# Kernel optimization log

Measured on AMD Instinct MI355X. Metric: run time of the kernel, lower is better.

## Reference

```python
import jax, jax.numpy as jnp
import numpy as np

B, S, HID = 2, 2048, 2048
NH, NKV, HD = 8, 2, 256
EPS = 1e-6
ROPE_THETA = 1e6


def _rms_norm(x, w):
    # Gemma3nRMSNorm: computed in fp32, x / sqrt(mean(x^2) + eps) * w
    xf = x.astype(jnp.float32)
    out = xf * jax.lax.rsqrt(jnp.mean(xf * xf, axis=-1, keepdims=True) + EPS) * w
    return out.astype(x.dtype)


def _rotate_half(x):
    x1, x2 = jnp.split(x, 2, axis=-1)
    return jnp.concatenate((-x2, x1), axis=-1)


def _apply_rope(x, cos, sin):
    # x: [B, S, H, D]; cos/sin: [B, S, D] -> unsqueeze head dim (unsqueeze_dim=2)
    c = cos[:, :, None, :]
    s = sin[:, :, None, :]
    return x * c + _rotate_half(x) * s


def setup_inputs() -> dict:
    key = jax.random.key(0)
    ks = jax.random.split(key, 6)
    hidden_states = jax.random.normal(ks[0], (B, S, HID), dtype=jnp.float32)
    # RoPE tables (theta = 1e6, Gemma3n)
    inv_freq = 1.0 / (ROPE_THETA ** (np.arange(0, HD, 2, dtype=np.float32) / HD))
    pos = np.arange(S, dtype=np.float32)
    freqs = pos[:, None] * inv_freq[None, :]            # [S, D/2]
    emb = np.concatenate([freqs, freqs], axis=-1)        # [S, D]
    cos = jnp.broadcast_to(jnp.asarray(np.cos(emb)), (B, S, HD)).astype(jnp.float32)
    sin = jnp.broadcast_to(jnp.asarray(np.sin(emb)), (B, S, HD)).astype(jnp.float32)
    # additive causal mask [B, 1, S, S]
    causal = jnp.tril(jnp.ones((S, S), dtype=bool))
    attention_mask = jnp.where(causal, 0.0, -1e9).astype(jnp.float32)
    attention_mask = jnp.broadcast_to(attention_mask[None, None], (B, 1, S, S))
    std = 0.02
    Wq = jax.random.normal(ks[1], (NH * HD, HID), dtype=jnp.float32) * std
    Wk = jax.random.normal(ks[2], (NKV * HD, HID), dtype=jnp.float32) * std
    Wv = jax.random.normal(ks[3], (NKV * HD, HID), dtype=jnp.float32) * std
    Wo = jax.random.normal(ks[4], (HID, NH * HD), dtype=jnp.float32) * std
    q_norm_w = jnp.ones((HD,), dtype=jnp.float32)
    k_norm_w = jnp.ones((HD,), dtype=jnp.float32)
    return {
        "hidden_states": hidden_states, "cos": cos, "sin": sin,
        "attention_mask": attention_mask,
        "Wq": Wq, "Wk": Wk, "Wv": Wv, "Wo": Wo,
        "q_norm_w": q_norm_w, "k_norm_w": k_norm_w,
    }


def reference(hidden_states, cos, sin, attention_mask, Wq, Wk, Wv, Wo, q_norm_w, k_norm_w):
    b, s, _ = hidden_states.shape
    # projections (no bias)
    q = (hidden_states @ Wq.T).reshape(b, s, NH, HD)
    k = (hidden_states @ Wk.T).reshape(b, s, NKV, HD)
    v = (hidden_states @ Wv.T).reshape(b, s, NKV, HD)
    # QK-norm then RoPE; v_norm has no scale (weight = 1)
    q = _apply_rope(_rms_norm(q, q_norm_w), cos, sin)
    k = _apply_rope(_rms_norm(k, k_norm_w), cos, sin)
    v = _rms_norm(v, jnp.float32(1.0))
    q = q.transpose(0, 2, 1, 3)  # [B, NH, S, D]
    k = k.transpose(0, 2, 1, 3)  # [B, NKV, S, D]
    v = v.transpose(0, 2, 1, 3)
    # repeat_kv: NKV -> NH (n_rep = NH // NKV)
    n_rep = NH // NKV
    k = jnp.repeat(k, n_rep, axis=1)
    v = jnp.repeat(v, n_rep, axis=1)
    # eager attention, scaling = 1.0 (as in Gemma3nTextAttention), no softcap
    scores = jnp.einsum("bhqd,bhkd->bhqk", q, k) + attention_mask
    probs = jax.nn.softmax(scores.astype(jnp.float32), axis=-1).astype(q.dtype)
    out = jnp.einsum("bhqk,bhkd->bqhd", probs, v).reshape(b, s, NH * HD)
    return out @ Wo.T
```

## Files before the change

kernel.cpp:

```cpp
#include <hip/hip_runtime.h>
#include <hip/hip_bf16.h>
#include <stdint.h>

#define S_LEN 2048
#define HIDN  2048
#define NH    8
#define NKV   2
#define HD    256

typedef _Float16 v8h  __attribute__((ext_vector_type(8)));
typedef float    v4f  __attribute__((ext_vector_type(4)));
typedef float    v16f __attribute__((ext_vector_type(16)));
typedef unsigned short u16;

struct alignas(8) US4 { u16 x, y, z, w; };

__device__ __forceinline__ u16 f2h(float f) {
  union { _Float16 h; u16 u; } t; t.h = (_Float16)f; return t.u;
}
__device__ __forceinline__ float h2f(u16 u) {
  union { _Float16 h; u16 u; } t; t.u = u; return (float)t.h;
}
__device__ __forceinline__ uint32_t pk2(float a, float b) {
  return (uint32_t)f2h(a) | ((uint32_t)f2h(b) << 16);
}

template <typename T>
__device__ __forceinline__ void gload16(const T* g, void* l) {
  __builtin_amdgcn_global_load_lds(
      (const __attribute__((address_space(1))) void*)g,
      (__attribute__((address_space(3))) void*)l, 16, 0, 0);
}

__global__ void cvt_h_kernel(const float* __restrict__ in, u16* __restrict__ out, int n4) {
  int i = blockIdx.x * blockDim.x + threadIdx.x;
  if (i >= n4) return;
  float4 v = reinterpret_cast<const float4*>(in)[i];
  US4 o; o.x = f2h(v.x); o.y = f2h(v.y); o.z = f2h(v.z); o.w = f2h(v.w);
  reinterpret_cast<US4*>(out)[i] = o;
}

__global__ __launch_bounds__(256, 2) void gemm_h_nt(
    const u16* __restrict__ A, const u16* __restrict__ Bm,
    float* __restrict__ C, int M, int N, int K) {
  __shared__ u16 As[128 * 32];
  __shared__ u16 Bs[128 * 32];
  const int tid = threadIdx.x;
  const int w = tid >> 6, lane = tid & 63;
  const int m0 = blockIdx.x * 128, n0 = blockIdx.y * 128;
  const int wr = (w >> 1) * 64, wc = (w & 1) * 64;
  const int lr = lane & 15, lk = (lane >> 4) << 3;
  v4f acc[4][4] = {};
  const int row1 = tid >> 2, col1 = (tid & 3) << 3;
  const int t2 = tid + 256;
  const int row2 = t2 >> 2, col2 = (t2 & 3) << 3;
  for (int kt = 0; kt < K; kt += 32) {
    __syncthreads();
    gload16(A  + (size_t)(m0 + row1) * K + kt + col1, (char*)As + tid * 16);
    gload16(Bm + (size_t)(n0 + row1) * K + kt + col1, (char*)Bs + tid * 16);
    gload16(A  + (size_t)(m0 + row2) * K + kt + col2, (char*)As + t2 * 16);
    gload16(Bm + (size_t)(n0 + row2) * K + kt + col2, (char*)Bs + t2 * 16);
    __syncthreads();
    v8h af[4], bfr[4];
#pragma unroll
    for (int i = 0; i < 4; i++) af[i]  = *reinterpret_cast<const v8h*>(&As[(wr + i * 16 + lr) * 32 + lk]);
#pragma unroll
    for (int i = 0; i < 4; i++) bfr[i] = *reinterpret_cast<const v8h*>(&Bs[(wc + i * 16 + lr) * 32 + lk]);
#pragma unroll
    for (int i = 0; i < 4; i++)
#pragma unroll
      for (int jn = 0; jn < 4; jn++)
        acc[i][jn] = __builtin_amdgcn_mfma_f32_16x16x32_f16(af[i], bfr[jn], acc[i][jn], 0, 0, 0);
  }
  const int rbase = m0 + wr + ((lane >> 4) << 2);
  const int cbase = n0 + wc + lr;
#pragma unroll
  for (int i = 0; i < 4; i++)
#pragma unroll
    for (int jn = 0; jn < 4; jn++) {
      const int col = cbase + jn * 16;
#pragma unroll
      for (int j = 0; j < 4; j++)
        C[(size_t)(rbase + i * 16 + j) * N + col] = acc[i][jn][j];
    }
}

__global__ __launch_bounds__(256, 4) void norm_rope_kernel(
    const float* __restrict__ qkv, const float* __restrict__ cosb, const float* __restrict__ sinb,
    const float* __restrict__ qw, const float* __restrict__ kw,
    u16* __restrict__ q_t, u16* __restrict__ k_t, u16* __restrict__ v_t) {
  const int task = blockIdx.x * 4 + (threadIdx.x >> 6);
  const int lane = threadIdx.x & 63;
  const int unit = task % 12;
  const int ms = task / 12;
  const int b = ms >> 11, s = ms & 2047;
  const int d0 = lane << 2;
  const int col0 = (unit < 8) ? unit * 256 : 2048 + (unit - 8) * 256;
  const float4 xv = *reinterpret_cast<const float4*>(qkv + (size_t)ms * 3072 + col0 + d0);
  float x[4] = { xv.x, xv.y, xv.z, xv.w };
  float ss = x[0]*x[0] + x[1]*x[1] + x[2]*x[2] + x[3]*x[3];
#pragma unroll
  for (int m = 1; m < 64; m <<= 1) ss += __shfl_xor(ss, m, 64);
  const float r = rsqrtf(ss * (1.0f / 256.0f) + 1e-6f);
  if (unit < 10) {
    const float4 wv = *reinterpret_cast<const float4*>(((unit < 8) ? qw : kw) + d0);
    float xn[4];
    xn[0] = x[0] * r * wv.x; xn[1] = x[1] * r * wv.y;
    xn[2] = x[2] * r * wv.z; xn[3] = x[3] * r * wv.w;
    float rot[4];
#pragma unroll
    for (int j = 0; j < 4; j++) {
      const float p = __shfl(xn[j], lane ^ 32, 64);
      rot[j] = (lane < 32) ? -p : p;
    }
    const float4 c  = *reinterpret_cast<const float4*>(cosb + (size_t)ms * 256 + d0);
    const float4 sn = *reinterpret_cast<const float4*>(sinb + (size_t)ms * 256 + d0);
    US4 o;
    o.x = f2h(xn[0] * c.x + rot[0] * sn.x);
    o.y = f2h(xn[1] * c.y + rot[1] * sn.y);
    o.z = f2h(xn[2] * c.z + rot[2] * sn.z);
    o.w = f2h(xn[3] * c.w + rot[3] * sn.w);
    if (unit < 8) {
      const size_t dst = ((size_t)(b * NH + unit) * S_LEN + s) * 256 + d0;
      *reinterpret_cast<US4*>(q_t + dst) = o;
    } else {
      const size_t dst = ((size_t)(b * NKV + (unit - 8)) * S_LEN + s) * 256 + d0;
      *reinterpret_cast<US4*>(k_t + dst) = o;
    }
  } else {
    const int kvh = unit - 10;
    u16* vt = v_t + (size_t)(b * NKV + kvh) * 256 * 2048;
#pragma unroll
    for (int j = 0; j < 4; j++)
      vt[(size_t)(d0 + j) * 2048 + s] = f2h(x[j] * r);
  }
}

__device__ __forceinline__ void stage_kv(
    const u16* __restrict__ kb, const u16* __restrict__ vb, int kt,
    u16* Kbuf, u16* Vbuf, int tid) {
#pragma unroll
  for (int it = 0; it < 4; it++) {
    const int i1 = tid + it * 512;
    const int kv = i1 >> 5, sp = i1 & 31;
    const int sl = sp ^ (kv & 31);
    gload16(kb + (size_t)(kt * 64 + kv) * 256 + sl * 8, (char*)Kbuf + i1 * 16);
    const int d = i1 >> 3, sp2 = i1 & 7;
    const int sl2 = sp2 ^ ((d >> 2) & 7);
    gload16(vb + (size_t)d * 2048 + kt * 64 + sl2 * 8, (char*)Vbuf + i1 * 16);
  }
}

__global__ __launch_bounds__(512, 2) void attn_kernel(
    const u16* __restrict__ q_t, const u16* __restrict__ k_t,
    const u16* __restrict__ v_t, u16* __restrict__ oP, float2* __restrict__ ml) {
  const int qtA = blockIdx.x;
  const int qtB = 15 - qtA;
  const int bh = blockIdx.y;
  const int b = bh >> 3, h = bh & 7, hk = h >> 2;
  const int tid = threadIdx.x;
  const int w = tid >> 6, lane = tid & 63;
  const int g = w >> 1, hf = w & 1;
  const int l31 = lane & 31, hi = lane >> 5;

  __shared__ u16 Kb[2][16384];
  __shared__ u16 Vb[2][16384];

  const u16* qhead = q_t + (size_t)(b * NH + h) * S_LEN * 256;
  const u16* kb = k_t + (size_t)(b * NKV + hk) * S_LEN * 256;
  const u16* vb = v_t + (size_t)(b * NKV + hk) * 256 * S_LEN;

  const u16* qbA = qhead + (size_t)(qtA * 128 + g * 32 + l31) * 256;
  v8h qf[16];
#pragma unroll
  for (int f = 0; f < 16; f++)
    qf[f] = *reinterpret_cast<const v8h*>(qbA + f * 16 + hi * 8);

  v16f o[4] = {};
  float mr = -1e30f, lsum = 0.f;
  int qt_cur = qtA;

  const int nA = qtA + 1;

  stage_kv(kb, vb, 0, Kb[0], Vb[0], tid);

  for (int s = 0; s < 17; s++) {
    const int cb = s & 1;
    const int kt = (s < nA) ? s : (qtB + 1 + s - nA);
    if (s + 1 < 17) {
      const int s1 = s + 1;
      const int ktn = (s1 < nA) ? s1 : (qtB + 1 + s1 - nA);
      stage_kv(kb, vb, ktn, Kb[cb ^ 1], Vb[cb ^ 1], tid);
      asm volatile("s_waitcnt vmcnt(8)" ::: "memory");
    } else {
      asm volatile("s_waitcnt vmcnt(0)" ::: "memory");
    }
    __builtin_amdgcn_s_barrier();
    __builtin_amdgcn_sched_barrier(0);

    if (s == nA) {
      const size_t rowi = (((size_t)bh) * 16 + qtA) * 128 + g * 32 + l31;
      u16* ob = oP + rowi * 256;
#pragma unroll
      for (int dblk = 0; dblk < 4; dblk++)
#pragma unroll
        for (int rr = 0; rr < 4; rr++) {
          const int dbase = hf * 128 + dblk * 32 + rr * 8 + hi * 4;
          uint2 pw;
          pw.x = pk2(o[dblk][rr * 4 + 0], o[dblk][rr * 4 + 1]);
          pw.y = pk2(o[dblk][rr * 4 + 2], o[dblk][rr * 4 + 3]);
          *reinterpret_cast<uint2*>(ob + dbase) = pw;
        }
      if (hf == 0 && lane < 32)
        ml[rowi] = make_float2(mr, lsum);
      const u16* qbB = qhead + (size_t)(qtB * 128 + g * 32 + l31) * 256;
#pragma unroll
      for (int f = 0; f < 16; f++)
        qf[f] = *reinterpret_cast<const v8h*>(qbB + f * 16 + hi * 8);
#pragma unroll
      for (int dblk = 0; dblk < 4; dblk++) o[dblk] = v16f{};
      mr = -1e30f; lsum = 0.f;
      qt_cur = qtB;
    }

    v16f s0 = {}, s1 = {};
    __builtin_amdgcn_s_setprio(1);
#pragma unroll
    for (int ds = 0; ds < 16; ds++) {
      const int sp = (ds * 2 + hi) ^ l31;
      const v8h kf0 = *reinterpret_cast<const v8h*>(&Kb[cb][l31 * 256 + sp * 8]);
      const v8h kf1 = *reinterpret_cast<const v8h*>(&Kb[cb][(32 + l31) * 256 + sp * 8]);
      s0 = __builtin_amdgcn_mfma_f32_32x32x16_f16(kf0, qf[ds], s0, 0, 0, 0);
      s1 = __builtin_amdgcn_mfma_f32_32x32x16_f16(kf1, qf[ds], s1, 0, 0, 0);
    }
    __builtin_amdgcn_s_setprio(0);
    if (kt >= 2 * qt_cur) {
      const int qg = qt_cur * 128 + g * 32 + l31;
#pragma unroll
      for (int r = 0; r < 16; r++) {
        const int kvr = kt * 64 + (r & 3) + 8 * (r >> 2) + 4 * hi;
        if (kvr > qg) s0[r] = -1e30f;
        if (kvr + 32 > qg) s1[r] = -1e30f;
      }
    }
    float pm = s0[0];
#pragma unroll
    for (int r = 1; r < 16; r++) pm = fmaxf(pm, s0[r]);
#pragma unroll
    for (int r = 0; r < 16; r++) pm = fmaxf(pm, s1[r]);
    pm = fmaxf(pm, __shfl_xor(pm, 32, 64));
    if (!__all(pm - mr <= 8.0f)) {
      const float mn = fmaxf(mr, pm);
      const float sc = __expf(mr - mn);
      mr = mn;
      lsum *= sc;
#pragma unroll
      for (int dblk = 0; dblk < 4; dblk++)
#pragma unroll
        for (int r = 0; r < 16; r++) o[dblk][r] *= sc;
    }
    float rs = 0.f;
#pragma unroll
    for (int r = 0; r < 16; r++) { s0[r] = __expf(s0[r] - mr); rs += s0[r]; }
#pragma unroll
    for (int r = 0; r < 16; r++) { s1[r] = __expf(s1[r] - mr); rs += s1[r]; }
    rs += __shfl_xor(rs, 32, 64);
    lsum += rs;
    uint32_t pka[2][8], pkx[2][8];
#pragma unroll
    for (int u = 0; u < 8; u++) {
      const int r = (u & 1) * 2 + (u >> 1) * 4;
      pka[0][u] = pk2(s0[r], s0[r + 1]);
      pka[1][u] = pk2(s1[r], s1[r + 1]);
    }
#pragma unroll
    for (int n = 0; n < 2; n++)
#pragma unroll
      for (int u = 0; u < 8; u++)
        pkx[n][u] = (uint32_t)__shfl_xor((int)pka[n][u], 32, 64);
    v8h bfr[4];
#pragma unroll
    for (int sblk = 0; sblk < 4; sblk++) {
      const int n = sblk >> 1, base = (sblk & 1) * 4;
      union { uint32_t u[4]; v8h h; } t;
      if (hi == 0) {
        t.u[0] = pka[n][base];     t.u[1] = pka[n][base + 1];
        t.u[2] = pkx[n][base];     t.u[3] = pkx[n][base + 1];
      } else {
        t.u[0] = pkx[n][base + 2]; t.u[1] = pkx[n][base + 3];
        t.u[2] = pka[n][base + 2]; t.u[3] = pka[n][base + 3];
      }
      bfr[sblk] = t.h;
    }
    __builtin_amdgcn_s_setprio(1);
#pragma unroll
    for (int dblk = 0; dblk < 4; dblk++) {
      const int d = hf * 128 + dblk * 32 + l31;
#pragma unroll
      for (int sblk = 0; sblk < 4; sblk++) {
        const int sp = (sblk * 2 + hi) ^ ((d >> 2) & 7);
        const v8h vf = *reinterpret_cast<const v8h*>(&Vb[cb][d * 64 + sp * 8]);
        o[dblk] = __builtin_amdgcn_mfma_f32_32x32x16_f16(vf, bfr[sblk], o[dblk], 0, 0, 0);
      }
    }
    __builtin_amdgcn_s_setprio(0);
    __builtin_amdgcn_s_barrier();
    __builtin_amdgcn_sched_barrier(0);
  }

  const size_t rowi = (((size_t)(16 + bh)) * 16 + qtB) * 128 + g * 32 + l31;
  u16* ob = oP + rowi * 256;
#pragma unroll
  for (int dblk = 0; dblk < 4; dblk++)
#pragma unroll
    for (int rr = 0; rr < 4; rr++) {
      const int dbase = hf * 128 + dblk * 32 + rr * 8 + hi * 4;
      uint2 pw;
      pw.x = pk2(o[dblk][rr * 4 + 0], o[dblk][rr * 4 + 1]);
      pw.y = pk2(o[dblk][rr * 4 + 2], o[dblk][rr * 4 + 3]);
      *reinterpret_cast<uint2*>(ob + dbase) = pw;
    }
  if (hf == 0 && lane < 32)
    ml[rowi] = make_float2(mr, lsum);
}

__global__ __launch_bounds__(256, 8) void combine_kernel(
    const u16* __restrict__ oP, const float2* __restrict__ ml,
    u16* __restrict__ aout) {
  const int wid = threadIdx.x >> 6, lane = threadIdx.x & 63;
  const int R = blockIdx.x * 4 + wid;
  const int bh = R >> 11, rem = R & 2047, qt = rem >> 7, row = rem & 127;
  const int b = bh >> 3, h = bh & 7;
  const size_t i0 = (((size_t)bh)      * 16 + qt) * 128 + row;
  const size_t i1 = (((size_t)(16+bh)) * 16 + qt) * 128 + row;
  const float2 m0 = ml[i0], m1 = ml[i1];
  const float ms = fmaxf(m0.x, m1.x);
  const float f0 = __expf(m0.x - ms), f1 = __expf(m1.x - ms);
  const float inv = 1.0f / (m0.y * f0 + m1.y * f1);
  const US4 a = reinterpret_cast<const US4*>(oP + i0 * 256)[lane];
  const US4 c = reinterpret_cast<const US4*>(oP + i1 * 256)[lane];
  US4 o;
  o.x = f2h((h2f(a.x) * f0 + h2f(c.x) * f1) * inv);
  o.y = f2h((h2f(a.y) * f0 + h2f(c.y) * f1) * inv);
  o.z = f2h((h2f(a.z) * f0 + h2f(c.z) * f1) * inv);
  o.w = f2h((h2f(a.w) * f0 + h2f(c.w) * f1) * inv);
  u16* dst = aout + ((size_t)(b * 2048 + qt * 128 + row)) * 2048 + h * 256 + lane * 4;
  *reinterpret_cast<US4*>(dst) = o;
}

extern "C" void kernel_launch(void* const* d_in, const int* in_sizes, int n_in,
                              void* d_out, int out_size, void* d_ws, size_t ws_size,
                              hipStream_t stream) {
  const float* hs   = (const float*)d_in[0];
  const float* cosb = (const float*)d_in[1];
  const float* sinb = (const float*)d_in[2];
  const float* Wq = (const float*)d_in[4];
  const float* Wk = (const float*)d_in[5];
  const float* Wv = (const float*)d_in[6];
  const float* Wo = (const float*)d_in[7];
  const float* qw = (const float*)d_in[8];
  const float* kw = (const float*)d_in[9];
  float* out = (float*)d_out;

  char* ws = (char*)d_ws;
  u16* hs_f = (u16*)(ws + 0);
  u16* w_f  = (u16*)(ws + 16777216);
  u16* wo_f = (u16*)(ws + 29360128);
  float* qkv = (float*)(ws + 37748736);
  u16* q_t  = (u16*)(ws + 88080384);
  u16* k_t  = (u16*)(ws + 104857600);
  u16* v_t  = (u16*)(ws + 109051904);
  u16* oP   = (u16*)(ws + 37748736);
  float2* mlp = (float2*)(ws + 71303168);
  u16* aout = (u16*)(ws + 0);

  cvt_h_kernel<<<8192, 256, 0, stream>>>(hs, hs_f, 2097152);
  cvt_h_kernel<<<4096, 256, 0, stream>>>(Wq, w_f,           1048576);
  cvt_h_kernel<<<1024, 256, 0, stream>>>(Wk, w_f + 4194304, 262144);
  cvt_h_kernel<<<1024, 256, 0, stream>>>(Wv, w_f + 5242880, 262144);
  cvt_h_kernel<<<4096, 256, 0, stream>>>(Wo, wo_f,          1048576);

  gemm_h_nt<<<dim3(32, 24), 256, 0, stream>>>(hs_f, w_f, qkv, 4096, 3072, 2048);
  norm_rope_kernel<<<12288, 256, 0, stream>>>(qkv, cosb, sinb, qw, kw, q_t, k_t, v_t);
  attn_kernel<<<dim3(16, 16), 512, 0, stream>>>(q_t, k_t, v_t, oP, mlp);
  combine_kernel<<<8192, 256, 0, stream>>>(oP, mlp, aout);
  gemm_h_nt<<<dim3(32, 16), 256, 0, stream>>>(aout, wo_f, out, 4096, 2048, 2048);
}
```

Measured before the change: 250.0 us.

## Replace GEMM with double-buffered swizzled 256-wide tiles and fp16 QKV output

The simple 128x128, K=32 GEMM is replaced by a templated kernel with 512 threads and 256x256 (QKV) or 128x256 (output) tiles. It uses K=64 steps, XOR-swizzled LDS layout, and double-buffered async global-to-LDS loads overlapped with MFMA phases using barriers and setprio. The QKV projection now writes fp16 instead of fp32, which halves the intermediate traffic read by norm_rope but adds rounding before the RMS norm. Larger tiles cut the global load count but leave fewer blocks in flight (192 and 256) on a device with many CUs.

```diff
diff --git a/kernel.cpp b/kernel.cpp
--- a/kernel.cpp
+++ b/kernel.cpp
@@ -40,53 +40,111 @@
   reinterpret_cast<US4*>(out)[i] = o;
 }
 
-__global__ __launch_bounds__(256, 2) void gemm_h_nt(
+template <int MF, int OUT_F16>
+__global__ __launch_bounds__(512, 2) void gemm256(
     const u16* __restrict__ A, const u16* __restrict__ Bm,
-    float* __restrict__ C, int M, int N, int K) {
-  __shared__ u16 As[128 * 32];
-  __shared__ u16 Bs[128 * 32];
+    void* __restrict__ C, int M, int N, int K) {
+  __shared__ u16 As[2][MF * 2048];
+  __shared__ u16 Bs[2][16384];
   const int tid = threadIdx.x;
   const int w = tid >> 6, lane = tid & 63;
-  const int m0 = blockIdx.x * 128, n0 = blockIdx.y * 128;
-  const int wr = (w >> 1) * 64, wc = (w & 1) * 64;
-  const int lr = lane & 15, lk = (lane >> 4) << 3;
-  v4f acc[4][4] = {};
-  const int row1 = tid >> 2, col1 = (tid & 3) << 3;
-  const int t2 = tid + 256;
-  const int row2 = t2 >> 2, col2 = (t2 & 3) << 3;
-  for (int kt = 0; kt < K; kt += 32) {
-    __syncthreads();
-    gload16(A  + (size_t)(m0 + row1) * K + kt + col1, (char*)As + tid * 16);
-    gload16(Bm + (size_t)(n0 + row1) * K + kt + col1, (char*)Bs + tid * 16);
-    gload16(A  + (size_t)(m0 + row2) * K + kt + col2, (char*)As + t2 * 16);
-    gload16(Bm + (size_t)(n0 + row2) * K + kt + col2, (char*)Bs + t2 * 16);
-    __syncthreads();
-    v8h af[4], bfr[4];
-#pragma unroll
-    for (int i = 0; i < 4; i++) af[i]  = *reinterpret_cast<const v8h*>(&As[(wr + i * 16 + lr) * 32 + lk]);
-#pragma unroll
-    for (int i = 0; i < 4; i++) bfr[i] = *reinterpret_cast<const v8h*>(&Bs[(wc + i * 16 + lr) * 32 + lk]);
-#pragma unroll
-    for (int i = 0; i < 4; i++)
-#pragma unroll
-      for (int jn = 0; jn < 4; jn++)
-        acc[i][jn] = __builtin_amdgcn_mfma_f32_16x16x32_f16(af[i], bfr[jn], acc[i][jn], 0, 0, 0);
+  const int wm = w >> 2, wn = w & 3;
+  const int lr = lane & 15, ls = lane >> 4;
+  const int m0 = blockIdx.x * (MF * 32);
+  const int n0 = blockIdx.y * 256;
+  const int KT = K >> 6;
+  constexpr int FPP = MF / 4;
+  v4f acc[MF][4] = {};
+
+  auto stageA = [&](int kt, int buf, int r) {
+    const int idx = r * 512 + tid;
+    const int row = idx >> 3, sp = idx & 7;
+    const int sl = sp ^ (row & 7);
+    gload16(A + (size_t)(m0 + row) * K + kt * 64 + sl * 8, (char*)As[buf] + idx * 16);
+  };
+  auto stageB = [&](int kt, int buf, int r) {
+    const int idx = r * 512 + tid;
+    const int row = idx >> 3, sp = idx & 7;
+    const int sl = sp ^ (row & 7);
+    gload16(Bm + (size_t)(n0 + row) * K + kt * 64 + sl * 8, (char*)Bs[buf] + idx * 16);
+  };
+
+#pragma unroll
+  for (int r = 0; r < MF / 2; r++) stageA(0, 0, r);
+#pragma unroll
+  for (int r = 0; r < 4; r++) stageB(0, 0, r);
+  asm volatile("s_waitcnt vmcnt(0)" ::: "memory");
+  __builtin_amdgcn_s_barrier();
+  __builtin_amdgcn_sched_barrier(0);
+
+  for (int kt = 0; kt < KT; kt++) {
+    const int buf = kt & 1;
+    v8h bfrag[2][4];
+#pragma unroll
+    for (int p = 0; p < 4; p++) {
+      if (p == 0) {
+#pragma unroll
+        for (int kk = 0; kk < 2; kk++)
+#pragma unroll
+          for (int j = 0; j < 4; j++) {
+            const int row = wn * 64 + j * 16 + lr;
+            const int sp = (kk * 4 + ls) ^ (row & 7);
+            bfrag[kk][j] = *reinterpret_cast<const v8h*>(&Bs[buf][row * 64 + sp * 8]);
+          }
+      }
+      v8h a2[FPP][2];
+#pragma unroll
+      for (int ii = 0; ii < FPP; ii++)
+#pragma unroll
+        for (int kk = 0; kk < 2; kk++) {
+          const int row = wm * MF * 16 + (p * FPP + ii) * 16 + lr;
+          const int sp = (kk * 4 + ls) ^ (row & 7);
+          a2[ii][kk] = *reinterpret_cast<const v8h*>(&As[buf][row * 64 + sp * 8]);
+        }
+      if (kt + 1 < KT) {
+        if (p == 0) {
+#pragma unroll
+          for (int r = 0; r < MF / 2; r++) stageA(kt + 1, buf ^ 1, r);
+        }
+        if (p == 1) {
+#pragma unroll
+          for (int r = 0; r < 4; r++) stageB(kt + 1, buf ^ 1, r);
+        }
+      }
+      if (p == 3) asm volatile("s_waitcnt vmcnt(0)" ::: "memory");
+      __builtin_amdgcn_s_barrier();
+      asm volatile("s_waitcnt lgkmcnt(0)" ::: "memory");
+      __builtin_amdgcn_sched_barrier(0);
+      __builtin_amdgcn_s_setprio(1);
+#pragma unroll
+      for (int ii = 0; ii < FPP; ii++)
+#pragma unroll
+        for (int j = 0; j < 4; j++)
+#pragma unroll
+          for (int kk = 0; kk < 2; kk++)
+            acc[p * FPP + ii][j] = __builtin_amdgcn_mfma_f32_16x16x32_f16(
+                a2[ii][kk], bfrag[kk][j], acc[p * FPP + ii][j], 0, 0, 0);
+      __builtin_amdgcn_s_setprio(0);
+      __builtin_amdgcn_s_barrier();
+    }
   }
-  const int rbase = m0 + wr + ((lane >> 4) << 2);
-  const int cbase = n0 + wc + lr;
-#pragma unroll
-  for (int i = 0; i < 4; i++)
-#pragma unroll
-    for (int jn = 0; jn < 4; jn++) {
-      const int col = cbase + jn * 16;
-#pragma unroll
-      for (int j = 0; j < 4; j++)
-        C[(size_t)(rbase + i * 16 + j) * N + col] = acc[i][jn][j];
+
+#pragma unroll
+  for (int i = 0; i < MF; i++)
+#pragma unroll
+    for (int j = 0; j < 4; j++) {
+      const int col = n0 + wn * 64 + j * 16 + lr;
+#pragma unroll
+      for (int jj = 0; jj < 4; jj++) {
+        const int row = m0 + wm * MF * 16 + i * 16 + ls * 4 + jj;
+        if (OUT_F16) ((u16*)C)[(size_t)row * N + col] = f2h(acc[i][j][jj]);
+        else         ((float*)C)[(size_t)row * N + col] = acc[i][j][jj];
+      }
     }
 }
 
 __global__ __launch_bounds__(256, 4) void norm_rope_kernel(
-    const float* __restrict__ qkv, const float* __restrict__ cosb, const float* __restrict__ sinb,
+    const u16* __restrict__ qkv, const float* __restrict__ cosb, const float* __restrict__ sinb,
     const float* __restrict__ qw, const float* __restrict__ kw,
     u16* __restrict__ q_t, u16* __restrict__ k_t, u16* __restrict__ v_t) {
   const int task = blockIdx.x * 4 + (threadIdx.x >> 6);
@@ -96,8 +154,8 @@
   const int b = ms >> 11, s = ms & 2047;
   const int d0 = lane << 2;
   const int col0 = (unit < 8) ? unit * 256 : 2048 + (unit - 8) * 256;
-  const float4 xv = *reinterpret_cast<const float4*>(qkv + (size_t)ms * 3072 + col0 + d0);
-  float x[4] = { xv.x, xv.y, xv.z, xv.w };
+  const US4 xv = *reinterpret_cast<const US4*>(qkv + (size_t)ms * 3072 + col0 + d0);
+  float x[4] = { h2f(xv.x), h2f(xv.y), h2f(xv.z), h2f(xv.w) };
   float ss = x[0]*x[0] + x[1]*x[1] + x[2]*x[2] + x[3]*x[3];
 #pragma unroll
   for (int m = 1; m < 64; m <<= 1) ss += __shfl_xor(ss, m, 64);
@@ -366,7 +424,7 @@
   u16* hs_f = (u16*)(ws + 0);
   u16* w_f  = (u16*)(ws + 16777216);
   u16* wo_f = (u16*)(ws + 29360128);
-  float* qkv = (float*)(ws + 37748736);
+  u16* qkvh = (u16*)(ws + 37748736);
   u16* q_t  = (u16*)(ws + 88080384);
   u16* k_t  = (u16*)(ws + 104857600);
   u16* v_t  = (u16*)(ws + 109051904);
@@ -380,9 +438,9 @@
   cvt_h_kernel<<<1024, 256, 0, stream>>>(Wv, w_f + 5242880, 262144);
   cvt_h_kernel<<<4096, 256, 0, stream>>>(Wo, wo_f,          1048576);
 
-  gemm_h_nt<<<dim3(32, 24), 256, 0, stream>>>(hs_f, w_f, qkv, 4096, 3072, 2048);
-  norm_rope_kernel<<<12288, 256, 0, stream>>>(qkv, cosb, sinb, qw, kw, q_t, k_t, v_t);
+  gemm256<8, 1><<<dim3(16, 12), 512, 0, stream>>>(hs_f, w_f, qkvh, 4096, 3072, 2048);
+  norm_rope_kernel<<<12288, 256, 0, stream>>>(qkvh, cosb, sinb, qw, kw, q_t, k_t, v_t);
   attn_kernel<<<dim3(16, 16), 512, 0, stream>>>(q_t, k_t, v_t, oP, mlp);
   combine_kernel<<<8192, 256, 0, stream>>>(oP, mlp, aout);
-  gemm_h_nt<<<dim3(32, 16), 256, 0, stream>>>(aout, wo_f, out, 4096, 2048, 2048);
-}
+  gemm256<4, 0><<<dim3(32, 8), 512, 0, stream>>>(aout, wo_f, out, 4096, 2048, 2048);
+}
```

Result: faster. 239.4 us (-4.3%).
